# Kernel tuning notes

Measured on AMD Instinct MI355X. Metric: run time of the kernel, lower is better.

The kernel has to match this reference:

```python
import jax, jax.numpy as jnp
import numpy as np
from jax import lax

B, C, H, W, K = 32, 128, 56, 56, 5
CR = C // 4          # reduced channels in weight-gen MLP
CE = 4 * C           # expanded channels
EPS = 1e-6


def setup_inputs() -> dict:
    key = jax.random.key(0)
    ks = jax.random.split(key, 8)
    s = lambda fan: 1.0 / np.sqrt(fan)
    return {
        "x": jax.random.normal(ks[0], (B, C, H, W), jnp.float32),
        "w_fc1": jax.random.normal(ks[1], (CR, C), jnp.float32) * s(C),
        "ln1_w": jnp.ones((CR,), jnp.float32),
        "ln1_b": jnp.zeros((CR,), jnp.float32),
        "w_fc2": jax.random.normal(ks[2], (C * K * K, CR), jnp.float32) * s(CR),
        "ln2_w": jnp.ones((C,), jnp.float32),
        "ln2_b": jnp.zeros((C,), jnp.float32),
        "w_expand": jax.random.normal(ks[3], (CE, C), jnp.float32) * s(C),
        "w_shrink": jax.random.normal(ks[4], (C, CE), jnp.float32) * s(CE),
        "grn_gamma": jax.random.normal(ks[5], (CE,), jnp.float32) * 0.1,
        "grn_beta": jax.random.normal(ks[6], (CE,), jnp.float32) * 0.1,
    }


def _ln(v, w, b, axis):
    u = v.mean(axis, keepdims=True)
    s2 = jnp.square(v - u).mean(axis, keepdims=True)
    return (v - u) * lax.rsqrt(s2 + EPS) * w + b


def reference(x, w_fc1, ln1_w, ln1_b, w_fc2, ln2_w, ln2_b, w_expand, w_shrink,
              grn_gamma, grn_beta):
    b, c, h, w = x.shape
    # ---- dynamic weight generation: pool -> fc1 -> LN -> fc2 ----
    pooled = x.mean((2, 3))                                  # [B, C]
    hdn = pooled @ w_fc1.T                                   # [B, CR]
    hdn = _ln(hdn, ln1_w, ln1_b, axis=-1)                    # channels_first LN over CR
    dyn = hdn @ w_fc2.T                                      # [B, C*K*K]
    dyn_w = dyn.reshape(b * c, 1, K, K)                      # per-sample depthwise kernels
    # ---- per-sample dynamic depthwise conv (groups = B*C) ----
    pad = K // 2
    out = lax.conv_general_dilated(
        x.reshape(1, b * c, h, w), dyn_w,
        window_strides=(1, 1), padding=[(pad, pad), (pad, pad)],
        dimension_numbers=("NCHW", "OIHW", "NCHW"),
        feature_group_count=b * c,
    ).reshape(b, c, h, w)
    # ---- LN (channels_first) over channel dim ----
    u = out.mean(1, keepdims=True)
    s2 = jnp.square(out - u).mean(1, keepdims=True)
    out = (out - u) * lax.rsqrt(s2 + EPS)
    out = ln2_w[None, :, None, None] * out + ln2_b[None, :, None, None]
    # ---- expand 1x1 -> GELU -> GRN -> shrink 1x1 ----
    out = jnp.einsum("bchw,oc->bohw", out, w_expand)         # [B, 4C, H, W]
    out = jax.nn.gelu(out, approximate=False)
    gx = jnp.sqrt(jnp.sum(jnp.square(out), axis=(2, 3), keepdims=True))  # [B,4C,1,1]
    nx = gx / (gx.mean(1, keepdims=True) + EPS)
    g = grn_gamma[None, :, None, None]
    bt = grn_beta[None, :, None, None]
    out = g * (out * nx) + bt + out
    out = jnp.einsum("bohw,co->bchw", out, w_shrink)         # [B, C, H, W]
    return out + x
```

## Files before the change

### kernel.cpp

```cpp
#include <hip/hip_runtime.h>
#include <hip/hip_bf16.h>

#define B_   32
#define C_   128
#define H_   56
#define W_   56
#define HW_  (H_*W_)
#define BHW_ (B_*HW_)
#define K5_  5
#define KK_  25
#define CR_  32
#define CE_  512
#define EPS_ 1e-6f

typedef __hip_bfloat16 bf16;
typedef __attribute__((ext_vector_type(8))) short short8;
typedef __attribute__((ext_vector_type(4))) float f32x4;


__device__ __forceinline__ float wave_reduce_sum(float v) {
#pragma unroll
  for (int off = 32; off > 0; off >>= 1) v += __shfl_down(v, off, 64);
  return v;
}
__device__ __forceinline__ float bf2f(unsigned short u) {
  return __uint_as_float(((unsigned)u) << 16);
}
__device__ __forceinline__ unsigned short f2bf_bits(float f) {
  bf16 h = __float2bfloat16(f);
  unsigned short u;
  __builtin_memcpy(&u, &h, 2);
  return u;
}
__device__ __forceinline__ float fast_gelu(float v) {
  float t = __expf(-1.702f * v);
  return v * __builtin_amdgcn_rcpf(1.0f + t);
}
__device__ __forceinline__ void glds16(const void* g, void* l) {
  __builtin_amdgcn_global_load_lds(
      (const __attribute__((address_space(1))) unsigned int*)g,
      (__attribute__((address_space(3))) unsigned int*)l, 16, 0, 0);
}

__global__ __launch_bounds__(256) void prep_kernel(const float* __restrict__ we,
                                                   const float* __restrict__ ws,
                                                   bf16* __restrict__ weB,
                                                   bf16* __restrict__ wsB,
                                                   float* __restrict__ gx2) {
  int i = blockIdx.x * 256 + threadIdx.x;
  if (i < CE_ * C_)          weB[i] = __float2bfloat16(we[i]);
  else if (i < 2 * CE_ * C_) wsB[i - CE_ * C_] = __float2bfloat16(ws[i - CE_ * C_]);
  else                       gx2[i - 2 * CE_ * C_] = 0.f;
}

__global__ __launch_bounds__(256) void pool_kernel(const float* __restrict__ x,
                                                   float* __restrict__ pooled) {
  int bc = blockIdx.x;
  const float4* xp4 = reinterpret_cast<const float4*>(x + (size_t)bc * HW_);
  float s = 0.f;
  for (int i = threadIdx.x; i < 784; i += 256) {
    float4 v = xp4[i];
    s += (v.x + v.y) + (v.z + v.w);
  }
  s = wave_reduce_sum(s);
  __shared__ float red[4];
  int lane = threadIdx.x & 63, wid = threadIdx.x >> 6;
  if (lane == 0) red[wid] = s;
  __syncthreads();
  if (threadIdx.x == 0) pooled[bc] = (red[0] + red[1] + red[2] + red[3]) * (1.0f / HW_);
}

__global__ __launch_bounds__(256) void fc_kernel(const float* __restrict__ pooled,
                                                 const float* __restrict__ w_fc1,
                                                 const float* __restrict__ ln1_w,
                                                 const float* __restrict__ ln1_b,
                                                 const float* __restrict__ w_fc2,
                                                 float* __restrict__ dyn) {
  int b = blockIdx.x;
  int tid = threadIdx.x;
  __shared__ float sp[C_];
  __shared__ float sh[CR_];
  __shared__ float shn[CR_];
  __shared__ float stats[2];
  if (tid < C_) sp[tid] = pooled[b * C_ + tid];
  __syncthreads();
  if (tid < CR_) {
    float acc = 0.f;
    const float* wr = w_fc1 + tid * C_;
#pragma unroll 4
    for (int c = 0; c < C_; ++c) acc += sp[c] * wr[c];
    sh[tid] = acc;
  }
  __syncthreads();
  if (tid == 0) {
    float u = 0.f;
    for (int j = 0; j < CR_; ++j) u += sh[j];
    u *= (1.0f / CR_);
    float v = 0.f;
    for (int j = 0; j < CR_; ++j) { float d = sh[j] - u; v += d * d; }
    v *= (1.0f / CR_);
    stats[0] = u;
    stats[1] = rsqrtf(v + EPS_);
  }
  __syncthreads();
  if (tid < CR_) shn[tid] = (sh[tid] - stats[0]) * stats[1] * ln1_w[tid] + ln1_b[tid];
  __syncthreads();
  for (int i = tid; i < C_ * KK_; i += 256) {
    const float* wr = w_fc2 + i * CR_;
    float acc = 0.f;
#pragma unroll
    for (int j = 0; j < CR_; ++j) acc += shn[j] * wr[j];
    dyn[b * (C_ * KK_) + i] = acc;
  }
}

__global__ __launch_bounds__(256) void conv_kernel(const float* __restrict__ x,
                                                   const float* __restrict__ dyn,
                                                   bf16* __restrict__ z) {
  int bc = blockIdx.x;
  int b = bc >> 7;
  int c = bc & 127;
  int tid = threadIdx.x;
  __shared__ float xs[(H_ + 4) * 64];
  __shared__ float wks[KK_];
  {
    int r = tid >> 6;
    int rr = (r < 2) ? r : (56 + r);
    xs[rr * 64 + (tid & 63)] = 0.f;
  }
  if (tid < 224) {
    int r = tid >> 2, q = tid & 3;
    int col = (q < 2) ? q : (56 + q);
    xs[(r + 2) * 64 + col] = 0.f;
  }
  if (tid < KK_) wks[tid] = dyn[b * (C_ * KK_) + c * KK_ + tid];
  const float4* xp4 = reinterpret_cast<const float4*>(x + (size_t)bc * HW_);
  for (int i = tid; i < 784; i += 256) {
    float4 v = xp4[i];
    int h = i / 14, w4 = (i % 14) * 4;
    float* dst = &xs[(h + 2) * 64 + 2 + w4];
    dst[0] = v.x; dst[1] = v.y; dst[2] = v.z; dst[3] = v.w;
  }
  __syncthreads();
  float wr[KK_];
#pragma unroll
  for (int j = 0; j < KK_; ++j) wr[j] = wks[j];
  for (int g = tid; g < 784; g += 256) {
    int h = g / 14;
    int w4 = (g % 14) * 4;
    float a0 = 0.f, a1 = 0.f, a2 = 0.f, a3 = 0.f;
#pragma unroll
    for (int dh = 0; dh < K5_; ++dh) {
      const float* row = &xs[(h + dh) * 64 + w4];
      float4 va = *reinterpret_cast<const float4*>(row);
      float4 vb = *reinterpret_cast<const float4*>(row + 4);
      float v0 = va.x, v1 = va.y, v2 = va.z, v3 = va.w;
      float v4 = vb.x, v5 = vb.y, v6 = vb.z, v7 = vb.w;
      float u0 = wr[dh * 5 + 0], u1 = wr[dh * 5 + 1], u2 = wr[dh * 5 + 2];
      float u3 = wr[dh * 5 + 3], u4 = wr[dh * 5 + 4];
      a0 += v0 * u0 + v1 * u1 + v2 * u2 + v3 * u3 + v4 * u4;
      a1 += v1 * u0 + v2 * u1 + v3 * u2 + v4 * u3 + v5 * u4;
      a2 += v2 * u0 + v3 * u1 + v4 * u2 + v5 * u3 + v6 * u4;
      a3 += v3 * u0 + v4 * u1 + v5 * u2 + v6 * u3 + v7 * u4;
    }
    size_t base = (size_t)bc * HW_ + h * W_ + w4;
    ushort4 pk = make_ushort4(f2bf_bits(a0), f2bf_bits(a1), f2bf_bits(a2), f2bf_bits(a3));
    *reinterpret_cast<ushort4*>(reinterpret_cast<unsigned short*>(z) + base) = pk;
  }
}

__global__ __launch_bounds__(256) void ln_kernel(const bf16* __restrict__ z,
                                                 const float* __restrict__ ln2_w,
                                                 const float* __restrict__ ln2_b,
                                                 bf16* __restrict__ yT) {
  int hw0 = blockIdx.x * 64;
  int b = blockIdx.y;
  int tid = threadIdx.x;
  int wq = tid & 63;
  int cq = tid >> 6;
  __shared__ unsigned short zt[C_][64];
  __shared__ unsigned short yt[64][136];
  __shared__ float redS[4][64];
  __shared__ float redQ[4][64];
  __shared__ float meanArr[64];
  __shared__ float invArr[64];
  const unsigned short* zp = reinterpret_cast<const unsigned short*>(z);
#pragma unroll
  for (int i = 0; i < 4; ++i) {
    int t = tid + 256 * i;
    int c = t >> 3, ch = t & 7;
    int4 v = *reinterpret_cast<const int4*>(zp + ((size_t)(b * C_ + c)) * HW_ + hw0 + ch * 8);
    *reinterpret_cast<int4*>(&zt[c][ch * 8]) = v;
  }
  __syncthreads();
  float s = 0.f, q = 0.f;
#pragma unroll 4
  for (int k = 0; k < 32; ++k) {
    float v = bf2f(zt[cq * 32 + k][wq]);
    s += v;
    q += v * v;
  }
  redS[cq][wq] = s;
  redQ[cq][wq] = q;
  __syncthreads();
  if (cq == 0) {
    float ss = redS[0][wq] + redS[1][wq] + redS[2][wq] + redS[3][wq];
    float qq = redQ[0][wq] + redQ[1][wq] + redQ[2][wq] + redQ[3][wq];
    float m = ss * (1.0f / C_);
    float var = qq * (1.0f / C_) - m * m;
    meanArr[wq] = m;
    invArr[wq] = rsqrtf(fmaxf(var, 0.f) + EPS_);
  }
  __syncthreads();
  float m = meanArr[wq], iv = invArr[wq];
#pragma unroll
  for (int g = 0; g < 4; ++g) {
    unsigned short pk[8];
#pragma unroll
    for (int i = 0; i < 8; ++i) {
      int c = cq * 32 + g * 8 + i;
      float v = bf2f(zt[c][wq]);
      pk[i] = f2bf_bits((v - m) * iv * ln2_w[c] + ln2_b[c]);
    }
    int4 t;
    __builtin_memcpy(&t, pk, 16);
    *reinterpret_cast<int4*>(&yt[wq][cq * 32 + g * 8]) = t;
  }
  __syncthreads();
  unsigned short* yp = reinterpret_cast<unsigned short*>(yT);
#pragma unroll
  for (int i = 0; i < 4; ++i) {
    int t = tid + 256 * i;
    int row = t >> 4, ch = t & 15;
    int4 v = *reinterpret_cast<const int4*>(&yt[row][ch * 8]);
    *reinterpret_cast<int4*>(yp + ((size_t)(b * HW_ + hw0 + row)) * C_ + ch * 8) = v;
  }
}

__global__ __launch_bounds__(256, 4) void expand_mfma(const bf16* __restrict__ yT,
                                                      const bf16* __restrict__ weB,
                                                      bf16* __restrict__ eT,
                                                      float* __restrict__ gx2) {
  int j0 = blockIdx.x * 128;
  int o0 = blockIdx.y * 128;
  int tid = threadIdx.x;
  int lane = tid & 63, wid = tid >> 6;
  int wm = wid >> 1, wn = wid & 1;
  int quad = lane >> 4, l15 = lane & 15;
  __shared__ __align__(16) char smem[34816];
  const short* yS = reinterpret_cast<const short*>(yT);
  const short* weS = reinterpret_cast<const short*>(weB);
  int sr = (wid * 2) * 16 + (lane >> 2);
  int scp = lane & 3;
  auto STAGE = [&](int bs, int k0) {
#pragma unroll
    for (int i = 0; i < 2; ++i) {
      int seg = wid * 2 + i;
      int r = sr + i * 16;
      int c = scp ^ ((r >> 1) & 3);
      char* base = smem + bs * 16384 + seg * 1024;
      glds16(yS + (size_t)(j0 + r) * C_ + k0 + c * 8, base);
      glds16(weS + (size_t)(o0 + r) * C_ + k0 + c * 8, base + 8192);
    }
  };
  f32x4 acc[4][4] = {};
  STAGE(0, 0);
  __syncthreads();
#pragma unroll
  for (int t = 0; t < 4; ++t) {
    if (t < 3) STAGE((t + 1) & 1, (t + 1) * 32);
    const char* ba = smem + (t & 1) * 16384;
    int sx = (quad ^ ((l15 >> 1) & 3)) * 16;
    short8 a[4], bfr[4];
#pragma unroll
    for (int mf = 0; mf < 4; ++mf)
      a[mf] = *reinterpret_cast<const short8*>(ba + (wm * 64 + mf * 16 + l15) * 64 + sx);
#pragma unroll
    for (int nf = 0; nf < 4; ++nf)
      bfr[nf] = *reinterpret_cast<const short8*>(ba + 8192 + (wn * 64 + nf * 16 + l15) * 64 + sx);
#pragma unroll
    for (int mf = 0; mf < 4; ++mf)
#pragma unroll
      for (int nf = 0; nf < 4; ++nf)
        acc[mf][nf] = __builtin_amdgcn_mfma_f32_16x16x32_bf16(a[mf], bfr[nf], acc[mf][nf], 0, 0, 0);
    __syncthreads();
  }
  short (*Es)[136] = reinterpret_cast<short(*)[136]>(&smem[0]);
#pragma unroll
  for (int mf = 0; mf < 4; ++mf) {
    int jm = j0 + wm * 64 + mf * 16;
    int bb = jm / HW_;
    int jrow = wm * 64 + mf * 16 + quad * 4;
#pragma unroll
    for (int nf = 0; nf < 4; ++nf) {
      int oc = wn * 64 + nf * 16 + l15;
      float g2 = 0.f;
#pragma unroll
      for (int r = 0; r < 4; ++r) {
        float ge = fast_gelu(acc[mf][nf][r]);
        g2 += ge * ge;
        Es[jrow + r][oc] = (short)f2bf_bits(ge);
      }
      g2 += __shfl_xor(g2, 16, 64);
      g2 += __shfl_xor(g2, 32, 64);
      if (quad == 0) atomicAdd(&gx2[bb * CE_ + o0 + oc], g2);
    }
  }
  __syncthreads();
  unsigned short* eP = reinterpret_cast<unsigned short*>(eT);
#pragma unroll
  for (int i = 0; i < 8; ++i) {
    int t = tid + 256 * i;
    int row = t >> 4, ch = t & 15;
    int4 v = *reinterpret_cast<const int4*>(&Es[row][ch * 8]);
    *reinterpret_cast<int4*>(eP + (size_t)(j0 + row) * CE_ + o0 + ch * 8) = v;
  }
}

__global__ __launch_bounds__(512) void grn_scale_kernel(const float* __restrict__ gx2,
                                                        const float* __restrict__ gamma,
                                                        float* __restrict__ scale) {
  int b = blockIdx.x;
  int o = threadIdx.x;
  float gx = sqrtf(gx2[b * CE_ + o]);
  float s = wave_reduce_sum(gx);
  __shared__ float red[8];
  __shared__ float meansh;
  int lane = o & 63, wid = o >> 6;
  if (lane == 0) red[wid] = s;
  __syncthreads();
  if (o == 0) {
    float t = 0.f;
    for (int i = 0; i < 8; ++i) t += red[i];
    meansh = t * (1.0f / CE_);
  }
  __syncthreads();
  scale[b * CE_ + o] = 1.0f + gamma[o] * (gx / (meansh + EPS_));
}

__global__ __launch_bounds__(256) void sb_kernel(const float* __restrict__ w_shrink,
                                                 const float* __restrict__ beta,
                                                 float* __restrict__ sb) {
  int c = blockIdx.x;
  const float* wp = w_shrink + (size_t)c * CE_;
  float acc = 0.f;
  for (int o = threadIdx.x; o < CE_; o += 256) acc += wp[o] * beta[o];
  acc = wave_reduce_sum(acc);
  __shared__ float red[4];
  int lane = threadIdx.x & 63, wid = threadIdx.x >> 6;
  if (lane == 0) red[wid] = acc;
  __syncthreads();
  if (threadIdx.x == 0) sb[c] = red[0] + red[1] + red[2] + red[3];
}

__global__ __launch_bounds__(256) void scale_ws_kernel(const float* __restrict__ ws,
                                                       const float* __restrict__ scale,
                                                       bf16* __restrict__ sws) {
  int c = blockIdx.x;
  int b = blockIdx.y;
  const float* sp = scale + b * CE_;
  const float* wp = ws + (size_t)c * CE_;
  bf16* op = sws + ((size_t)(b * C_ + c)) * CE_;
  for (int i = threadIdx.x; i < CE_; i += 256)
    op[i] = __float2bfloat16(wp[i] * sp[i]);
}

__global__ __launch_bounds__(256, 3) void shrink_mfma(const bf16* __restrict__ eT,
                                                      const bf16* __restrict__ sws,
                                                      const float* __restrict__ sb,
                                                      const float* __restrict__ x,
                                                      float* __restrict__ out) {
  int hw0 = blockIdx.x * 64;
  int b = blockIdx.y;
  int tid = threadIdx.x;
  int lane = tid & 63, wid = tid >> 6;
  int wm = wid >> 1, wn = wid & 1;
  int quad = lane >> 4, l15 = lane & 15;
  __shared__ __align__(16) char smem[49152];
  const short* eS  = reinterpret_cast<const short*>(eT) + (size_t)b * HW_ * CE_;
  const short* wsS = reinterpret_cast<const short*>(sws) + (size_t)b * C_ * CE_;
  int lr = lane >> 3;
  int lc = lane & 7;
  auto STAGE = [&](int bs, int k0) {
    char* base = smem + bs * 24576;
#pragma unroll
    for (int i = 0; i < 2; ++i) {
      int seg = wid * 2 + i;
      int r = seg * 8 + lr;
      int c = lc ^ (r & 7);
      glds16(eS + (size_t)(hw0 + r) * CE_ + k0 + c * 8, base + seg * 1024);
    }
#pragma unroll
    for (int i = 0; i < 4; ++i) {
      int seg = wid * 4 + i;
      int r = seg * 8 + lr;
      int c = lc ^ (r & 7);
      glds16(wsS + (size_t)r * CE_ + k0 + c * 8, base + 8192 + seg * 1024);
    }
  };
  f32x4 acc[2][4] = {};
  STAGE(0, 0);
  __syncthreads();
#pragma unroll 1
  for (int t = 0; t < 8; ++t) {
    if (t < 7) STAGE((t + 1) & 1, (t + 1) * 64);
    const char* ba = smem + (t & 1) * 24576;
#pragma unroll
    for (int ks = 0; ks < 2; ++ks) {
      short8 a[2], bfr[4];
#pragma unroll
      for (int mf = 0; mf < 2; ++mf) {
        int row = wm * 32 + mf * 16 + l15;
        int cp = (ks * 4 + quad) ^ (row & 7);
        a[mf] = *reinterpret_cast<const short8*>(ba + row * 128 + cp * 16);
      }
#pragma unroll
      for (int nf = 0; nf < 4; ++nf) {
        int row = wn * 64 + nf * 16 + l15;
        int cp = (ks * 4 + quad) ^ (row & 7);
        bfr[nf] = *reinterpret_cast<const short8*>(ba + 8192 + row * 128 + cp * 16);
      }
#pragma unroll
      for (int mf = 0; mf < 2; ++mf)
#pragma unroll
        for (int nf = 0; nf < 4; ++nf)
          acc[mf][nf] = __builtin_amdgcn_mfma_f32_16x16x32_bf16(a[mf], bfr[nf], acc[mf][nf], 0, 0, 0);
    }
    __syncthreads();
  }
  float (*Ef)[68] = reinterpret_cast<float(*)[68]>(&smem[0]);
#pragma unroll
  for (int mf = 0; mf < 2; ++mf) {
    int hwr = wm * 32 + mf * 16 + quad * 4;
#pragma unroll
    for (int nf = 0; nf < 4; ++nf)
      *reinterpret_cast<f32x4*>(&Ef[wn * 64 + nf * 16 + l15][hwr]) = acc[mf][nf];
  }
  __syncthreads();
#pragma unroll
  for (int i = 0; i < 8; ++i) {
    int t = tid + 256 * i;
    int row = t >> 4, ch = t & 15;
    int hw = hw0 + ch * 4;
    size_t base = ((size_t)(b * C_ + row)) * HW_ + hw;
    float add = sb[row];
    f32x4 av = *reinterpret_cast<const f32x4*>(&Ef[row][ch * 4]);
    float4 xv = *reinterpret_cast<const float4*>(x + base);
    float4 ov;
    ov.x = av.x + add + xv.x;
    ov.y = av.y + add + xv.y;
    ov.z = av.z + add + xv.z;
    ov.w = av.w + add + xv.w;
    *reinterpret_cast<float4*>(out + base) = ov;
  }
}

extern "C" void kernel_launch(void* const* d_in, const int* in_sizes, int n_in,
                              void* d_out, int out_size, void* d_ws, size_t ws_size,
                              hipStream_t stream) {
  (void)in_sizes; (void)n_in; (void)out_size; (void)ws_size;
  const float* x        = (const float*)d_in[0];
  const float* w_fc1    = (const float*)d_in[1];
  const float* ln1_w    = (const float*)d_in[2];
  const float* ln1_b    = (const float*)d_in[3];
  const float* w_fc2    = (const float*)d_in[4];
  const float* ln2_w    = (const float*)d_in[5];
  const float* ln2_b    = (const float*)d_in[6];
  const float* w_expand = (const float*)d_in[7];
  const float* w_shrink = (const float*)d_in[8];
  const float* gamma    = (const float*)d_in[9];
  const float* beta     = (const float*)d_in[10];
  float* out = (float*)d_out;

  char* ws = (char*)d_ws;
  float* pooled = (float*)(ws + 0);
  float* dyn    = (float*)(ws + 16384);
  float* gx2    = (float*)(ws + 425984);
  float* scale  = (float*)(ws + 491520);
  float* sb     = (float*)(ws + 557056);
  bf16*  weB    = (bf16*)(ws + 557568);
  bf16*  wsB    = (bf16*)(ws + 688640);
  bf16*  yT     = (bf16*)(ws + 819712);
  bf16*  sws    = (bf16*)(ws + 819712);
  bf16*  eT     = (bf16*)(ws + 26509824);
  bf16*  z      = eT;

  prep_kernel<<<576, 256, 0, stream>>>(w_expand, w_shrink, weB, wsB, gx2);
  sb_kernel<<<C_, 256, 0, stream>>>(w_shrink, beta, sb);
  pool_kernel<<<B_ * C_, 256, 0, stream>>>(x, pooled);
  fc_kernel<<<B_, 256, 0, stream>>>(pooled, w_fc1, ln1_w, ln1_b, w_fc2, dyn);
  conv_kernel<<<B_ * C_, 256, 0, stream>>>(x, dyn, z);
  ln_kernel<<<dim3(49, B_), 256, 0, stream>>>(z, ln2_w, ln2_b, yT);
  expand_mfma<<<dim3(784, 4), 256, 0, stream>>>(yT, weB, eT, gx2);
  grn_scale_kernel<<<B_, 512, 0, stream>>>(gx2, gamma, scale);
  scale_ws_kernel<<<dim3(C_, B_), 256, 0, stream>>>(w_shrink, scale, sws);
  shrink_mfma<<<dim3(49, B_), 256, 0, stream>>>(eT, sws, sb, x, out);
}
```

Measured before the change: 264.3 us.

## Merge prep kernels, fuse GRN scale into weight scaling, swizzle expand epilogue LDS

Three small setup kernels (weight conversion, shrink-bias, pooling) become one launch, and the GRN scale kernel is folded into the per-batch shrink-weight scaling kernel, which cuts launch count and drops the scale buffer round-trip. In exchange, every (c,b) block recomputes the per-batch GRN mean. The expand epilogue staging buffer switches from a padded layout to an XOR-swizzled one so it fits in 32 KB, and expand's launch bounds rise to 5 blocks per CU to allow more occupancy. That may push register pressure or cause spills.

```diff
diff --git a/kernel.cpp b/kernel.cpp
--- a/kernel.cpp
+++ b/kernel.cpp
@@ -42,32 +42,47 @@
       (__attribute__((address_space(3))) unsigned int*)l, 16, 0, 0);
 }
 
-__global__ __launch_bounds__(256) void prep_kernel(const float* __restrict__ we,
-                                                   const float* __restrict__ ws,
-                                                   bf16* __restrict__ weB,
-                                                   bf16* __restrict__ wsB,
-                                                   float* __restrict__ gx2) {
-  int i = blockIdx.x * 256 + threadIdx.x;
-  if (i < CE_ * C_)          weB[i] = __float2bfloat16(we[i]);
-  else if (i < 2 * CE_ * C_) wsB[i - CE_ * C_] = __float2bfloat16(ws[i - CE_ * C_]);
-  else                       gx2[i - 2 * CE_ * C_] = 0.f;
-}
-
-__global__ __launch_bounds__(256) void pool_kernel(const float* __restrict__ x,
-                                                   float* __restrict__ pooled) {
-  int bc = blockIdx.x;
-  const float4* xp4 = reinterpret_cast<const float4*>(x + (size_t)bc * HW_);
-  float s = 0.f;
-  for (int i = threadIdx.x; i < 784; i += 256) {
-    float4 v = xp4[i];
-    s += (v.x + v.y) + (v.z + v.w);
-  }
-  s = wave_reduce_sum(s);
-  __shared__ float red[4];
-  int lane = threadIdx.x & 63, wid = threadIdx.x >> 6;
-  if (lane == 0) red[wid] = s;
-  __syncthreads();
-  if (threadIdx.x == 0) pooled[bc] = (red[0] + red[1] + red[2] + red[3]) * (1.0f / HW_);
+__global__ __launch_bounds__(256) void prep_all(const float* __restrict__ we,
+                                                const float* __restrict__ ws,
+                                                const float* __restrict__ beta,
+                                                const float* __restrict__ x,
+                                                bf16* __restrict__ weB,
+                                                bf16* __restrict__ wsB,
+                                                float* __restrict__ gx2,
+                                                float* __restrict__ sb,
+                                                float* __restrict__ pooled) {
+  int bx = blockIdx.x;
+  if (bx < 576) {
+    int i = bx * 256 + threadIdx.x;
+    if (i < CE_ * C_)          weB[i] = __float2bfloat16(we[i]);
+    else if (i < 2 * CE_ * C_) wsB[i - CE_ * C_] = __float2bfloat16(ws[i - CE_ * C_]);
+    else                       gx2[i - 2 * CE_ * C_] = 0.f;
+  } else if (bx < 704) {
+    int c = bx - 576;
+    const float* wp = ws + (size_t)c * CE_;
+    float acc = 0.f;
+    for (int o = threadIdx.x; o < CE_; o += 256) acc += wp[o] * beta[o];
+    acc = wave_reduce_sum(acc);
+    __shared__ float red[4];
+    int lane = threadIdx.x & 63, wid = threadIdx.x >> 6;
+    if (lane == 0) red[wid] = acc;
+    __syncthreads();
+    if (threadIdx.x == 0) sb[c] = red[0] + red[1] + red[2] + red[3];
+  } else {
+    int bc = bx - 704;
+    const float4* xp4 = reinterpret_cast<const float4*>(x + (size_t)bc * HW_);
+    float s = 0.f;
+    for (int i = threadIdx.x; i < 784; i += 256) {
+      float4 v = xp4[i];
+      s += (v.x + v.y) + (v.z + v.w);
+    }
+    s = wave_reduce_sum(s);
+    __shared__ float redp[4];
+    int lane = threadIdx.x & 63, wid = threadIdx.x >> 6;
+    if (lane == 0) redp[wid] = s;
+    __syncthreads();
+    if (threadIdx.x == 0) pooled[bc] = (redp[0] + redp[1] + redp[2] + redp[3]) * (1.0f / HW_);
+  }
 }
 
 __global__ __launch_bounds__(256) void fc_kernel(const float* __restrict__ pooled,
@@ -237,7 +252,7 @@
   }
 }
 
-__global__ __launch_bounds__(256, 4) void expand_mfma(const bf16* __restrict__ yT,
+__global__ __launch_bounds__(256, 5) void expand_mfma(const bf16* __restrict__ yT,
                                                       const bf16* __restrict__ weB,
                                                       bf16* __restrict__ eT,
                                                       float* __restrict__ gx2) {
@@ -247,7 +262,7 @@
   int lane = tid & 63, wid = tid >> 6;
   int wm = wid >> 1, wn = wid & 1;
   int quad = lane >> 4, l15 = lane & 15;
-  __shared__ __align__(16) char smem[34816];
+  __shared__ __align__(16) char smem[32768];
   const short* yS = reinterpret_cast<const short*>(yT);
   const short* weS = reinterpret_cast<const short*>(weB);
   int sr = (wid * 2) * 16 + (lane >> 2);
@@ -285,7 +300,7 @@
         acc[mf][nf] = __builtin_amdgcn_mfma_f32_16x16x32_bf16(a[mf], bfr[nf], acc[mf][nf], 0, 0, 0);
     __syncthreads();
   }
-  short (*Es)[136] = reinterpret_cast<short(*)[136]>(&smem[0]);
+  unsigned short* Ep = reinterpret_cast<unsigned short*>(smem);
 #pragma unroll
   for (int mf = 0; mf < 4; ++mf) {
     int jm = j0 + wm * 64 + mf * 16;
@@ -294,12 +309,14 @@
 #pragma unroll
     for (int nf = 0; nf < 4; ++nf) {
       int oc = wn * 64 + nf * 16 + l15;
+      int lchunk = oc >> 3, lrem = oc & 7;
       float g2 = 0.f;
 #pragma unroll
       for (int r = 0; r < 4; ++r) {
         float ge = fast_gelu(acc[mf][nf][r]);
         g2 += ge * ge;
-        Es[jrow + r][oc] = (short)f2bf_bits(ge);
+        int row = jrow + r;
+        Ep[row * 128 + ((lchunk ^ (row & 15)) << 3) + lrem] = f2bf_bits(ge);
       }
       g2 += __shfl_xor(g2, 16, 64);
       g2 += __shfl_xor(g2, 32, 64);
@@ -312,57 +329,40 @@
   for (int i = 0; i < 8; ++i) {
     int t = tid + 256 * i;
     int row = t >> 4, ch = t & 15;
-    int4 v = *reinterpret_cast<const int4*>(&Es[row][ch * 8]);
+    int4 v = *reinterpret_cast<const int4*>(Ep + row * 128 + ((ch ^ (row & 15)) << 3));
     *reinterpret_cast<int4*>(eP + (size_t)(j0 + row) * CE_ + o0 + ch * 8) = v;
   }
 }
 
-__global__ __launch_bounds__(512) void grn_scale_kernel(const float* __restrict__ gx2,
-                                                        const float* __restrict__ gamma,
-                                                        float* __restrict__ scale) {
-  int b = blockIdx.x;
-  int o = threadIdx.x;
-  float gx = sqrtf(gx2[b * CE_ + o]);
-  float s = wave_reduce_sum(gx);
-  __shared__ float red[8];
-  __shared__ float meansh;
-  int lane = o & 63, wid = o >> 6;
-  if (lane == 0) red[wid] = s;
-  __syncthreads();
-  if (o == 0) {
-    float t = 0.f;
-    for (int i = 0; i < 8; ++i) t += red[i];
-    meansh = t * (1.0f / CE_);
-  }
-  __syncthreads();
-  scale[b * CE_ + o] = 1.0f + gamma[o] * (gx / (meansh + EPS_));
-}
-
-__global__ __launch_bounds__(256) void sb_kernel(const float* __restrict__ w_shrink,
-                                                 const float* __restrict__ beta,
-                                                 float* __restrict__ sb) {
-  int c = blockIdx.x;
-  const float* wp = w_shrink + (size_t)c * CE_;
-  float acc = 0.f;
-  for (int o = threadIdx.x; o < CE_; o += 256) acc += wp[o] * beta[o];
-  acc = wave_reduce_sum(acc);
-  __shared__ float red[4];
-  int lane = threadIdx.x & 63, wid = threadIdx.x >> 6;
-  if (lane == 0) red[wid] = acc;
-  __syncthreads();
-  if (threadIdx.x == 0) sb[c] = red[0] + red[1] + red[2] + red[3];
-}
-
-__global__ __launch_bounds__(256) void scale_ws_kernel(const float* __restrict__ ws,
-                                                       const float* __restrict__ scale,
-                                                       bf16* __restrict__ sws) {
+__global__ __launch_bounds__(256) void grn_scale_ws(const float* __restrict__ gx2,
+                                                    const float* __restrict__ gamma,
+                                                    const float* __restrict__ ws,
+                                                    bf16* __restrict__ sws) {
   int c = blockIdx.x;
   int b = blockIdx.y;
-  const float* sp = scale + b * CE_;
+  int tid = threadIdx.x;
+  __shared__ float gxs[CE_];
+  __shared__ float red[4];
+  __shared__ float invm;
+  const float* gp = gx2 + b * CE_;
+  float g0 = sqrtf(gp[tid]);
+  float g1 = sqrtf(gp[tid + 256]);
+  gxs[tid] = g0;
+  gxs[tid + 256] = g1;
+  float s = wave_reduce_sum(g0 + g1);
+  int lane = tid & 63, wid = tid >> 6;
+  if (lane == 0) red[wid] = s;
+  __syncthreads();
+  if (tid == 0) invm = 1.0f / ((red[0] + red[1] + red[2] + red[3]) * (1.0f / CE_) + EPS_);
+  __syncthreads();
+  float im = invm;
   const float* wp = ws + (size_t)c * CE_;
   bf16* op = sws + ((size_t)(b * C_ + c)) * CE_;
-  for (int i = threadIdx.x; i < CE_; i += 256)
-    op[i] = __float2bfloat16(wp[i] * sp[i]);
+#pragma unroll
+  for (int i = tid; i < CE_; i += 256) {
+    float sc = 1.0f + gamma[i] * (gxs[i] * im);
+    op[i] = __float2bfloat16(wp[i] * sc);
+  }
 }
 
 __global__ __launch_bounds__(256, 3) void shrink_mfma(const bf16* __restrict__ eT,
@@ -476,7 +476,6 @@
   float* pooled = (float*)(ws + 0);
   float* dyn    = (float*)(ws + 16384);
   float* gx2    = (float*)(ws + 425984);
-  float* scale  = (float*)(ws + 491520);
   float* sb     = (float*)(ws + 557056);
   bf16*  weB    = (bf16*)(ws + 557568);
   bf16*  wsB    = (bf16*)(ws + 688640);
@@ -485,14 +484,11 @@
   bf16*  eT     = (bf16*)(ws + 26509824);
   bf16*  z      = eT;
 
-  prep_kernel<<<576, 256, 0, stream>>>(w_expand, w_shrink, weB, wsB, gx2);
-  sb_kernel<<<C_, 256, 0, stream>>>(w_shrink, beta, sb);
-  pool_kernel<<<B_ * C_, 256, 0, stream>>>(x, pooled);
+  prep_all<<<4800, 256, 0, stream>>>(w_expand, w_shrink, beta, x, weB, wsB, gx2, sb, pooled);
   fc_kernel<<<B_, 256, 0, stream>>>(pooled, w_fc1, ln1_w, ln1_b, w_fc2, dyn);
   conv_kernel<<<B_ * C_, 256, 0, stream>>>(x, dyn, z);
   ln_kernel<<<dim3(49, B_), 256, 0, stream>>>(z, ln2_w, ln2_b, yT);
   expand_mfma<<<dim3(784, 4), 256, 0, stream>>>(yT, weB, eT, gx2);
-  grn_scale_kernel<<<B_, 512, 0, stream>>>(gx2, gamma, scale);
-  scale_ws_kernel<<<dim3(C_, B_), 256, 0, stream>>>(w_shrink, scale, sws);
+  grn_scale_ws<<<dim3(C_, B_), 256, 0, stream>>>(gx2, gamma, w_shrink, sws);
   shrink_mfma<<<dim3(49, B_), 256, 0, stream>>>(eT, sws, sb, x, out);
 }
```

Result: slower. 286.9 us (+8.6%).
